# Kernel optimization log

Hardware: AMD Instinct MI355X
Metric: run time of the kernel (lower is better)

The kernel has to match this reference:

```python
import jax, jax.numpy as jnp
import numpy as np

# --- instant-NGP style multiresolution hash grid config ---
N_LEVELS = 16
F = 2                      # features per level
LOG2_T = 19
T = 1 << LOG2_T            # hash table size per level
BASE_RES = 16
SCALE = 1.5
RES = np.floor(BASE_RES * SCALE ** np.arange(N_LEVELS)).astype(np.int64)
OFFSETS = np.array([[i, j, k] for i in (0, 1) for j in (0, 1) for k in (0, 1)], dtype=np.uint32)  # [8,3] cube corners
PRIMES = np.array([1, 2654435761, 805459861], dtype=np.uint32)  # tcnn spatial hash primes
N_PTS = 2_097_152


def hash_encode(x, table):
    """x: [N,3] in [0,1); table: [L,T,F] -> [N, L*F] interpolated features."""
    feats = []
    for l in range(N_LEVELS):  # fixed small loop over levels
        res = int(RES[l])
        pos = x * res
        pos0 = jnp.floor(pos)
        w = pos - pos0                                   # [N,3] trilinear weights
        c = pos0.astype(jnp.uint32)[:, None, :] + OFFSETS[None]  # [N,8,3] corner coords
        if (res + 1) ** 3 <= T:
            # dense indexing when the full grid fits in the table
            s = np.uint32(res + 1)
            idx = c[..., 0] + c[..., 1] * s + c[..., 2] * s * s
        else:
            # spatial hash: xor of coord * prime, mod T (uint32 wraps)
            idx = (c[..., 0] * PRIMES[0]) ^ (c[..., 1] * PRIMES[1]) ^ (c[..., 2] * PRIMES[2])
            idx = idx % np.uint32(T)
        f = table[l][idx]                                # [N,8,F] irregular gather
        wc = jnp.where(OFFSETS[None].astype(bool), w[:, None, :], 1.0 - w[:, None, :])  # [N,8,3]
        weight = wc.prod(axis=-1)                        # [N,8]
        feats.append(jnp.einsum('nc,ncf->nf', weight, f))
    return jnp.concatenate(feats, axis=-1)               # [N, 32]


def setup_inputs() -> dict:
    key = jax.random.key(0)
    k1, k2, k3, k4, k5 = jax.random.split(key, 5)
    x = jax.random.uniform(k1, (N_PTS, 3), dtype=jnp.float32)
    table = jax.random.normal(k2, (N_LEVELS, T, F), dtype=jnp.float32) * 1e-2
    W1 = jax.random.normal(k3, (N_LEVELS * F, 64), dtype=jnp.float32) * (1.0 / np.sqrt(32))
    W2 = jax.random.normal(k4, (64, 64), dtype=jnp.float32) * (1.0 / 8.0)
    W3 = jax.random.normal(k5, (64, 16), dtype=jnp.float32) * (1.0 / 8.0)
    return {"x": x, "table": table, "W1": W1, "W2": W2, "W3": W3}


def reference(x, table, W1, W2, W3):
    h = hash_encode(x, table)           # [N,32]
    h = jax.nn.relu(h @ W1)             # fully-fused tiny MLP (bias-free, tcnn style)
    h = jax.nn.relu(h @ W2)
    return h @ W3                        # [N,16]
```

## Files before the change

### kernel.cpp

```cpp
#include <hip/hip_runtime.h>
#include <hip/hip_bf16.h>


#define NLVL 16
#define TSZ   524288u
#define TMASK 524287u
#define PR1 2654435761u
#define PR2 805459861u

__device__ __constant__ int kResC[NLVL] = {16,24,36,54,81,121,182,273,410,615,922,1383,2075,3113,4670,7006};
constexpr int kRes[NLVL] = {16,24,36,54,81,121,182,273,410,615,922,1383,2075,3113,4670,7006};
constexpr bool kDense[NLVL] = {true,true,true,true,false,false,false,false,
                               false,false,false,false,false,false,false,false};

__global__ __launch_bounds__(256)
void ngp_fused_kernel(const float* __restrict__ x,
                      const float* __restrict__ table,
                      const float* __restrict__ W1,
                      const float* __restrict__ W2,
                      const float* __restrict__ W3,
                      float* __restrict__ out,
                      int n)
{
    __shared__ float sW1[32 * 64];
    __shared__ float sW2[64 * 64];
    __shared__ float sW3[64 * 16];
    __shared__ float hS[32 * 256];

    const int t = threadIdx.x;

#pragma unroll
    for (int r = 0; r < 8; ++r)  sW1[r * 256 + t] = W1[r * 256 + t];
#pragma unroll
    for (int r = 0; r < 16; ++r) sW2[r * 256 + t] = W2[r * 256 + t];
#pragma unroll
    for (int r = 0; r < 4; ++r)  sW3[r * 256 + t] = W3[r * 256 + t];
    __syncthreads();

    const int i = blockIdx.x * 256 + t;
    if (i >= n) return;

    const float px = x[3 * i + 0];
    const float py = x[3 * i + 1];
    const float pz = x[3 * i + 2];

    float h[32];
#pragma unroll
    for (int l = 0; l < NLVL; ++l) {
        const float res = (float)kRes[l];
        const float fx = px * res, fy = py * res, fz = pz * res;
        const float bx = floorf(fx), by = floorf(fy), bz = floorf(fz);
        const float wx = fx - bx, wy = fy - by, wz = fz - bz;
        const unsigned cx = (unsigned)bx, cy = (unsigned)by, cz = (unsigned)bz;

        unsigned i0, i1, i2, i3, i4, i5, i6, i7;
        if (kDense[l]) {
            const unsigned s  = (unsigned)kRes[l] + 1u;
            const unsigned s2 = s * s;
            const unsigned b  = cx + cy * s + cz * s2;
            i0 = b;            i1 = b + s2;
            i2 = b + s;        i3 = b + s + s2;
            i4 = b + 1u;       i5 = b + 1u + s2;
            i6 = b + 1u + s;   i7 = b + 1u + s + s2;
        } else {
            const unsigned hx0 = cx,        hx1 = cx + 1u;
            const unsigned hy0 = cy * PR1,  hy1 = hy0 + PR1;
            const unsigned hz0 = cz * PR2,  hz1 = hz0 + PR2;
            i0 = (hx0 ^ hy0 ^ hz0) & TMASK;  i1 = (hx0 ^ hy0 ^ hz1) & TMASK;
            i2 = (hx0 ^ hy1 ^ hz0) & TMASK;  i3 = (hx0 ^ hy1 ^ hz1) & TMASK;
            i4 = (hx1 ^ hy0 ^ hz0) & TMASK;  i5 = (hx1 ^ hy0 ^ hz1) & TMASK;
            i6 = (hx1 ^ hy1 ^ hz0) & TMASK;  i7 = (hx1 ^ hy1 ^ hz1) & TMASK;
        }

        const float2* __restrict__ tl =
            reinterpret_cast<const float2*>(table) + (size_t)l * TSZ;
        const float2 f0 = tl[i0], f1 = tl[i1], f2 = tl[i2], f3 = tl[i3];
        const float2 f4 = tl[i4], f5 = tl[i5], f6 = tl[i6], f7 = tl[i7];

        const float ax = 1.f - wx, ay = 1.f - wy, az = 1.f - wz;
        const float g00 = ax * ay, g01 = ax * wy, g10 = wx * ay, g11 = wx * wy;
        float a0 = 0.f, a1 = 0.f, v;
        v = g00 * az; a0 = fmaf(v, f0.x, a0); a1 = fmaf(v, f0.y, a1);
        v = g00 * wz; a0 = fmaf(v, f1.x, a0); a1 = fmaf(v, f1.y, a1);
        v = g01 * az; a0 = fmaf(v, f2.x, a0); a1 = fmaf(v, f2.y, a1);
        v = g01 * wz; a0 = fmaf(v, f3.x, a0); a1 = fmaf(v, f3.y, a1);
        v = g10 * az; a0 = fmaf(v, f4.x, a0); a1 = fmaf(v, f4.y, a1);
        v = g10 * wz; a0 = fmaf(v, f5.x, a0); a1 = fmaf(v, f5.y, a1);
        v = g11 * az; a0 = fmaf(v, f6.x, a0); a1 = fmaf(v, f6.y, a1);
        v = g11 * wz; a0 = fmaf(v, f7.x, a0); a1 = fmaf(v, f7.y, a1);
        h[2 * l + 0] = a0;
        h[2 * l + 1] = a1;
    }

#pragma unroll
    for (int k = 0; k < 32; ++k) hS[k * 256 + t] = h[k];

    float h1[64];
#pragma unroll
    for (int j = 0; j < 64; ++j) h1[j] = 0.f;
    for (int k = 0; k < 32; ++k) {
        const float hk = hS[k * 256 + t];
        const float4* __restrict__ wr = reinterpret_cast<const float4*>(&sW1[k * 64]);
#pragma unroll
        for (int q = 0; q < 16; ++q) {
            const float4 wv = wr[q];
            h1[4 * q + 0] = fmaf(hk, wv.x, h1[4 * q + 0]);
            h1[4 * q + 1] = fmaf(hk, wv.y, h1[4 * q + 1]);
            h1[4 * q + 2] = fmaf(hk, wv.z, h1[4 * q + 2]);
            h1[4 * q + 3] = fmaf(hk, wv.w, h1[4 * q + 3]);
        }
    }
#pragma unroll
    for (int j = 0; j < 64; ++j) h1[j] = fmaxf(h1[j], 0.f);

    float h2[64];
#pragma unroll
    for (int j = 0; j < 64; ++j) h2[j] = 0.f;

#pragma unroll
    for (int k = 0; k < 32; ++k) hS[k * 256 + t] = h1[k];
    for (int k = 0; k < 32; ++k) {
        const float hk = hS[k * 256 + t];
        const float4* __restrict__ wr = reinterpret_cast<const float4*>(&sW2[k * 64]);
#pragma unroll
        for (int q = 0; q < 16; ++q) {
            const float4 wv = wr[q];
            h2[4 * q + 0] = fmaf(hk, wv.x, h2[4 * q + 0]);
            h2[4 * q + 1] = fmaf(hk, wv.y, h2[4 * q + 1]);
            h2[4 * q + 2] = fmaf(hk, wv.z, h2[4 * q + 2]);
            h2[4 * q + 3] = fmaf(hk, wv.w, h2[4 * q + 3]);
        }
    }
#pragma unroll
    for (int k = 0; k < 32; ++k) hS[k * 256 + t] = h1[32 + k];
    for (int k = 0; k < 32; ++k) {
        const float hk = hS[k * 256 + t];
        const float4* __restrict__ wr = reinterpret_cast<const float4*>(&sW2[(k + 32) * 64]);
#pragma unroll
        for (int q = 0; q < 16; ++q) {
            const float4 wv = wr[q];
            h2[4 * q + 0] = fmaf(hk, wv.x, h2[4 * q + 0]);
            h2[4 * q + 1] = fmaf(hk, wv.y, h2[4 * q + 1]);
            h2[4 * q + 2] = fmaf(hk, wv.z, h2[4 * q + 2]);
            h2[4 * q + 3] = fmaf(hk, wv.w, h2[4 * q + 3]);
        }
    }
#pragma unroll
    for (int j = 0; j < 64; ++j) h2[j] = fmaxf(h2[j], 0.f);

    float h3[16];
#pragma unroll
    for (int j = 0; j < 16; ++j) h3[j] = 0.f;

#pragma unroll
    for (int k = 0; k < 32; ++k) hS[k * 256 + t] = h2[k];
    for (int k = 0; k < 32; ++k) {
        const float hk = hS[k * 256 + t];
        const float4* __restrict__ wr = reinterpret_cast<const float4*>(&sW3[k * 16]);
#pragma unroll
        for (int q = 0; q < 4; ++q) {
            const float4 wv = wr[q];
            h3[4 * q + 0] = fmaf(hk, wv.x, h3[4 * q + 0]);
            h3[4 * q + 1] = fmaf(hk, wv.y, h3[4 * q + 1]);
            h3[4 * q + 2] = fmaf(hk, wv.z, h3[4 * q + 2]);
            h3[4 * q + 3] = fmaf(hk, wv.w, h3[4 * q + 3]);
        }
    }
#pragma unroll
    for (int k = 0; k < 32; ++k) hS[k * 256 + t] = h2[32 + k];
    for (int k = 0; k < 32; ++k) {
        const float hk = hS[k * 256 + t];
        const float4* __restrict__ wr = reinterpret_cast<const float4*>(&sW3[(k + 32) * 16]);
#pragma unroll
        for (int q = 0; q < 4; ++q) {
            const float4 wv = wr[q];
            h3[4 * q + 0] = fmaf(hk, wv.x, h3[4 * q + 0]);
            h3[4 * q + 1] = fmaf(hk, wv.y, h3[4 * q + 1]);
            h3[4 * q + 2] = fmaf(hk, wv.z, h3[4 * q + 2]);
            h3[4 * q + 3] = fmaf(hk, wv.w, h3[4 * q + 3]);
        }
    }

    float4* __restrict__ o = reinterpret_cast<float4*>(out + (size_t)i * 16);
    o[0] = make_float4(h3[0],  h3[1],  h3[2],  h3[3]);
    o[1] = make_float4(h3[4],  h3[5],  h3[6],  h3[7]);
    o[2] = make_float4(h3[8],  h3[9],  h3[10], h3[11]);
    o[3] = make_float4(h3[12], h3[13], h3[14], h3[15]);
}

extern "C" void kernel_launch(void* const* d_in, const int* in_sizes, int n_in,
                              void* d_out, int out_size, void* d_ws, size_t ws_size,
                              hipStream_t stream) {
    const float* x     = (const float*)d_in[0];
    const float* table = (const float*)d_in[1];
    const float* W1    = (const float*)d_in[2];
    const float* W2    = (const float*)d_in[3];
    const float* W3    = (const float*)d_in[4];
    float* out = (float*)d_out;

    const int n = in_sizes[0] / 3;
    const int blocks = (n + 255) / 256;
    ngp_fused_kernel<<<blocks, 256, 0, stream>>>(x, table, W1, W2, W3, out, n);
}
```

Before: 1.697 ms.

## Split into level-major encode kernel and separate register-resident MLP kernel

Encoding moves into its own kernel whose grid is partitioned by level, one pass for the four dense levels and one per hash level, so concurrently running blocks gather from a single 4 MB table and get better L2 locality. Features are written to a feature-major workspace, and a second kernel runs the MLP from registers, chaining layer 2 and layer 3 in halves and dropping the LDS round-trips. This adds 256 MB of workspace write plus read traffic and a second launch. The old fused kernel remains as a fallback when the workspace is too small. The grid is hardcoded to 4096 chunks of 512 points, which matches exactly N=2M.

```diff
diff --git a/kernel.cpp b/kernel.cpp
--- a/kernel.cpp
+++ b/kernel.cpp
@@ -12,6 +12,208 @@
 constexpr int kRes[NLVL] = {16,24,36,54,81,121,182,273,410,615,922,1383,2075,3113,4670,7006};
 constexpr bool kDense[NLVL] = {true,true,true,true,false,false,false,false,
                                false,false,false,false,false,false,false,false};
+
+
+__device__ __forceinline__ void trilerp(const float2 f0, const float2 f1, const float2 f2, const float2 f3,
+                                        const float2 f4, const float2 f5, const float2 f6, const float2 f7,
+                                        float wx, float wy, float wz, float& a0, float& a1)
+{
+    const float ax = 1.f - wx, ay = 1.f - wy, az = 1.f - wz;
+    const float g00 = ax * ay, g01 = ax * wy, g10 = wx * ay, g11 = wx * wy;
+    float s0 = 0.f, s1 = 0.f, v;
+    v = g00 * az; s0 = fmaf(v, f0.x, s0); s1 = fmaf(v, f0.y, s1);
+    v = g00 * wz; s0 = fmaf(v, f1.x, s0); s1 = fmaf(v, f1.y, s1);
+    v = g01 * az; s0 = fmaf(v, f2.x, s0); s1 = fmaf(v, f2.y, s1);
+    v = g01 * wz; s0 = fmaf(v, f3.x, s0); s1 = fmaf(v, f3.y, s1);
+    v = g10 * az; s0 = fmaf(v, f4.x, s0); s1 = fmaf(v, f4.y, s1);
+    v = g10 * wz; s0 = fmaf(v, f5.x, s0); s1 = fmaf(v, f5.y, s1);
+    v = g11 * az; s0 = fmaf(v, f6.x, s0); s1 = fmaf(v, f6.y, s1);
+    v = g11 * wz; s0 = fmaf(v, f7.x, s0); s1 = fmaf(v, f7.y, s1);
+    a0 = s0; a1 = s1;
+}
+
+__device__ __forceinline__ void hash_point(float px, float py, float pz, float res,
+                                           const float2* __restrict__ tl,
+                                           float& a0, float& a1)
+{
+    const float fx = px * res, fy = py * res, fz = pz * res;
+    const float bx = floorf(fx), by = floorf(fy), bz = floorf(fz);
+    const float wx = fx - bx, wy = fy - by, wz = fz - bz;
+    const unsigned cx = (unsigned)bx, cy = (unsigned)by, cz = (unsigned)bz;
+    const unsigned hy0 = cy * PR1, hy1 = hy0 + PR1;
+    const unsigned hz0 = cz * PR2, hz1 = hz0 + PR2;
+    const unsigned e00 = hy0 ^ hz0, e01 = hy0 ^ hz1, e10 = hy1 ^ hz0, e11 = hy1 ^ hz1;
+    const unsigned x1 = cx + 1u;
+    const float2 f0 = tl[(cx ^ e00) & TMASK];
+    const float2 f1 = tl[(cx ^ e01) & TMASK];
+    const float2 f2 = tl[(cx ^ e10) & TMASK];
+    const float2 f3 = tl[(cx ^ e11) & TMASK];
+    const float2 f4 = tl[(x1 ^ e00) & TMASK];
+    const float2 f5 = tl[(x1 ^ e01) & TMASK];
+    const float2 f6 = tl[(x1 ^ e10) & TMASK];
+    const float2 f7 = tl[(x1 ^ e11) & TMASK];
+    trilerp(f0,f1,f2,f3,f4,f5,f6,f7, wx,wy,wz, a0,a1);
+}
+
+template<int RES>
+__device__ __forceinline__ void dense_point(float px, float py, float pz,
+                                            const float2* __restrict__ tl,
+                                            float& a0, float& a1)
+{
+    const float res = (float)RES;
+    const float fx = px * res, fy = py * res, fz = pz * res;
+    const float bx = floorf(fx), by = floorf(fy), bz = floorf(fz);
+    const float wx = fx - bx, wy = fy - by, wz = fz - bz;
+    const unsigned cx = (unsigned)bx, cy = (unsigned)by, cz = (unsigned)bz;
+    const unsigned s = RES + 1u, s2 = s * s;
+    const unsigned b = cx + cy * s + cz * s2;
+    const float2 f0 = tl[b];
+    const float2 f1 = tl[b + s2];
+    const float2 f2 = tl[b + s];
+    const float2 f3 = tl[b + s + s2];
+    const float2 f4 = tl[b + 1u];
+    const float2 f5 = tl[b + 1u + s2];
+    const float2 f6 = tl[b + 1u + s];
+    const float2 f7 = tl[b + 1u + s + s2];
+    trilerp(f0,f1,f2,f3,f4,f5,f6,f7, wx,wy,wz, a0,a1);
+}
+
+__global__ __launch_bounds__(256)
+void encode_kernel(const float* __restrict__ x, const float* __restrict__ table,
+                   float* __restrict__ hT, int n)
+{
+    const int bid = blockIdx.x;
+    const int pass = bid >> 12;
+    const int chunk = bid & 4095;
+    const int t = threadIdx.x;
+    const int base = chunk * 512 + t;
+
+    if (pass == 0) {
+#pragma unroll
+        for (int p = 0; p < 2; ++p) {
+            const int i = base + p * 256;
+            if (i >= n) continue;
+            const float px = x[3*i+0], py = x[3*i+1], pz = x[3*i+2];
+            float a0, a1;
+            dense_point<16>(px,py,pz, (const float2*)table + (size_t)0*TSZ, a0,a1);
+            hT[(size_t)0*n + i] = a0; hT[(size_t)1*n + i] = a1;
+            dense_point<24>(px,py,pz, (const float2*)table + (size_t)1*TSZ, a0,a1);
+            hT[(size_t)2*n + i] = a0; hT[(size_t)3*n + i] = a1;
+            dense_point<36>(px,py,pz, (const float2*)table + (size_t)2*TSZ, a0,a1);
+            hT[(size_t)4*n + i] = a0; hT[(size_t)5*n + i] = a1;
+            dense_point<54>(px,py,pz, (const float2*)table + (size_t)3*TSZ, a0,a1);
+            hT[(size_t)6*n + i] = a0; hT[(size_t)7*n + i] = a1;
+        }
+    } else {
+        const int l = pass + 3;
+        const float res = (float)kResC[l];
+        const float2* tl = (const float2*)table + (size_t)l * TSZ;
+        float* __restrict__ r0 = hT + (size_t)(2*l) * n;
+        float* __restrict__ r1 = r0 + n;
+#pragma unroll
+        for (int p = 0; p < 2; ++p) {
+            const int i = base + p * 256;
+            if (i >= n) continue;
+            const float px = x[3*i+0], py = x[3*i+1], pz = x[3*i+2];
+            float a0, a1;
+            hash_point(px,py,pz, res, tl, a0,a1);
+            r0[i] = a0; r1[i] = a1;
+        }
+    }
+}
+
+
+__global__ __launch_bounds__(256)
+void mlp_kernel(const float* __restrict__ hT,
+                const float* __restrict__ W1,
+                const float* __restrict__ W2,
+                const float* __restrict__ W3,
+                float* __restrict__ out, int n)
+{
+    __shared__ float sW1[32 * 64];
+    __shared__ float sW2[64 * 64];
+    __shared__ float sW3[64 * 16];
+    const int t = threadIdx.x;
+#pragma unroll
+    for (int r = 0; r < 8; ++r)  sW1[r * 256 + t] = W1[r * 256 + t];
+#pragma unroll
+    for (int r = 0; r < 16; ++r) sW2[r * 256 + t] = W2[r * 256 + t];
+#pragma unroll
+    for (int r = 0; r < 4; ++r)  sW3[r * 256 + t] = W3[r * 256 + t];
+    __syncthreads();
+
+    const int i = blockIdx.x * 256 + t;
+    if (i >= n) return;
+
+    float h[32];
+#pragma unroll
+    for (int f = 0; f < 32; ++f) h[f] = hT[(size_t)f * n + i];
+
+    float h1[64];
+#pragma unroll
+    for (int j = 0; j < 64; ++j) h1[j] = 0.f;
+#pragma unroll
+    for (int k = 0; k < 32; ++k) {
+        const float hk = h[k];
+        const float4* __restrict__ wr = reinterpret_cast<const float4*>(&sW1[k * 64]);
+#pragma unroll
+        for (int q = 0; q < 16; ++q) {
+            const float4 wv = wr[q];
+            h1[4*q+0] = fmaf(hk, wv.x, h1[4*q+0]);
+            h1[4*q+1] = fmaf(hk, wv.y, h1[4*q+1]);
+            h1[4*q+2] = fmaf(hk, wv.z, h1[4*q+2]);
+            h1[4*q+3] = fmaf(hk, wv.w, h1[4*q+3]);
+        }
+    }
+#pragma unroll
+    for (int j = 0; j < 64; ++j) h1[j] = fmaxf(h1[j], 0.f);
+
+    float h3[16];
+#pragma unroll
+    for (int j = 0; j < 16; ++j) h3[j] = 0.f;
+
+#pragma unroll
+    for (int half = 0; half < 2; ++half) {
+        float h2[32];
+#pragma unroll
+        for (int j = 0; j < 32; ++j) h2[j] = 0.f;
+#pragma unroll
+        for (int k = 0; k < 64; ++k) {
+            const float hk = h1[k];
+            const float4* __restrict__ wr = reinterpret_cast<const float4*>(&sW2[k * 64 + half * 32]);
+#pragma unroll
+            for (int q = 0; q < 8; ++q) {
+                const float4 wv = wr[q];
+                h2[4*q+0] = fmaf(hk, wv.x, h2[4*q+0]);
+                h2[4*q+1] = fmaf(hk, wv.y, h2[4*q+1]);
+                h2[4*q+2] = fmaf(hk, wv.z, h2[4*q+2]);
+                h2[4*q+3] = fmaf(hk, wv.w, h2[4*q+3]);
+            }
+        }
+#pragma unroll
+        for (int j = 0; j < 32; ++j) h2[j] = fmaxf(h2[j], 0.f);
+#pragma unroll
+        for (int k = 0; k < 32; ++k) {
+            const float hk = h2[k];
+            const float4* __restrict__ wr = reinterpret_cast<const float4*>(&sW3[(half * 32 + k) * 16]);
+#pragma unroll
+            for (int q = 0; q < 4; ++q) {
+                const float4 wv = wr[q];
+                h3[4*q+0] = fmaf(hk, wv.x, h3[4*q+0]);
+                h3[4*q+1] = fmaf(hk, wv.y, h3[4*q+1]);
+                h3[4*q+2] = fmaf(hk, wv.z, h3[4*q+2]);
+                h3[4*q+3] = fmaf(hk, wv.w, h3[4*q+3]);
+            }
+        }
+    }
+
+    float4* __restrict__ o = reinterpret_cast<float4*>(out + (size_t)i * 16);
+    o[0] = make_float4(h3[0],  h3[1],  h3[2],  h3[3]);
+    o[1] = make_float4(h3[4],  h3[5],  h3[6],  h3[7]);
+    o[2] = make_float4(h3[8],  h3[9],  h3[10], h3[11]);
+    o[3] = make_float4(h3[12], h3[13], h3[14], h3[15]);
+}
+
 
 __global__ __launch_bounds__(256)
 void ngp_fused_kernel(const float* __restrict__ x,
@@ -28,7 +230,6 @@
     __shared__ float hS[32 * 256];
 
     const int t = threadIdx.x;
-
 #pragma unroll
     for (int r = 0; r < 8; ++r)  sW1[r * 256 + t] = W1[r * 256 + t];
 #pragma unroll
@@ -40,56 +241,22 @@
     const int i = blockIdx.x * 256 + t;
     if (i >= n) return;
 
-    const float px = x[3 * i + 0];
-    const float py = x[3 * i + 1];
-    const float pz = x[3 * i + 2];
+    const float px = x[3*i+0], py = x[3*i+1], pz = x[3*i+2];
 
     float h[32];
 #pragma unroll
     for (int l = 0; l < NLVL; ++l) {
-        const float res = (float)kRes[l];
-        const float fx = px * res, fy = py * res, fz = pz * res;
-        const float bx = floorf(fx), by = floorf(fy), bz = floorf(fz);
-        const float wx = fx - bx, wy = fy - by, wz = fz - bz;
-        const unsigned cx = (unsigned)bx, cy = (unsigned)by, cz = (unsigned)bz;
-
-        unsigned i0, i1, i2, i3, i4, i5, i6, i7;
+        float a0, a1;
         if (kDense[l]) {
-            const unsigned s  = (unsigned)kRes[l] + 1u;
-            const unsigned s2 = s * s;
-            const unsigned b  = cx + cy * s + cz * s2;
-            i0 = b;            i1 = b + s2;
-            i2 = b + s;        i3 = b + s + s2;
-            i4 = b + 1u;       i5 = b + 1u + s2;
-            i6 = b + 1u + s;   i7 = b + 1u + s + s2;
+            const int r = kRes[l];
+            if (r == 16) dense_point<16>(px,py,pz,(const float2*)table+(size_t)l*TSZ,a0,a1);
+            else if (r == 24) dense_point<24>(px,py,pz,(const float2*)table+(size_t)l*TSZ,a0,a1);
+            else if (r == 36) dense_point<36>(px,py,pz,(const float2*)table+(size_t)l*TSZ,a0,a1);
+            else dense_point<54>(px,py,pz,(const float2*)table+(size_t)l*TSZ,a0,a1);
         } else {
-            const unsigned hx0 = cx,        hx1 = cx + 1u;
-            const unsigned hy0 = cy * PR1,  hy1 = hy0 + PR1;
-            const unsigned hz0 = cz * PR2,  hz1 = hz0 + PR2;
-            i0 = (hx0 ^ hy0 ^ hz0) & TMASK;  i1 = (hx0 ^ hy0 ^ hz1) & TMASK;
-            i2 = (hx0 ^ hy1 ^ hz0) & TMASK;  i3 = (hx0 ^ hy1 ^ hz1) & TMASK;
-            i4 = (hx1 ^ hy0 ^ hz0) & TMASK;  i5 = (hx1 ^ hy0 ^ hz1) & TMASK;
-            i6 = (hx1 ^ hy1 ^ hz0) & TMASK;  i7 = (hx1 ^ hy1 ^ hz1) & TMASK;
-        }
-
-        const float2* __restrict__ tl =
-            reinterpret_cast<const float2*>(table) + (size_t)l * TSZ;
-        const float2 f0 = tl[i0], f1 = tl[i1], f2 = tl[i2], f3 = tl[i3];
-        const float2 f4 = tl[i4], f5 = tl[i5], f6 = tl[i6], f7 = tl[i7];
-
-        const float ax = 1.f - wx, ay = 1.f - wy, az = 1.f - wz;
-        const float g00 = ax * ay, g01 = ax * wy, g10 = wx * ay, g11 = wx * wy;
-        float a0 = 0.f, a1 = 0.f, v;
-        v = g00 * az; a0 = fmaf(v, f0.x, a0); a1 = fmaf(v, f0.y, a1);
-        v = g00 * wz; a0 = fmaf(v, f1.x, a0); a1 = fmaf(v, f1.y, a1);
-        v = g01 * az; a0 = fmaf(v, f2.x, a0); a1 = fmaf(v, f2.y, a1);
-        v = g01 * wz; a0 = fmaf(v, f3.x, a0); a1 = fmaf(v, f3.y, a1);
-        v = g10 * az; a0 = fmaf(v, f4.x, a0); a1 = fmaf(v, f4.y, a1);
-        v = g10 * wz; a0 = fmaf(v, f5.x, a0); a1 = fmaf(v, f5.y, a1);
-        v = g11 * az; a0 = fmaf(v, f6.x, a0); a1 = fmaf(v, f6.y, a1);
-        v = g11 * wz; a0 = fmaf(v, f7.x, a0); a1 = fmaf(v, f7.y, a1);
-        h[2 * l + 0] = a0;
-        h[2 * l + 1] = a1;
+            hash_point(px,py,pz,(float)kRes[l],(const float2*)table+(size_t)l*TSZ,a0,a1);
+        }
+        h[2*l+0] = a0; h[2*l+1] = a1;
     }
 
 #pragma unroll
@@ -104,10 +271,10 @@
 #pragma unroll
         for (int q = 0; q < 16; ++q) {
             const float4 wv = wr[q];
-            h1[4 * q + 0] = fmaf(hk, wv.x, h1[4 * q + 0]);
-            h1[4 * q + 1] = fmaf(hk, wv.y, h1[4 * q + 1]);
-            h1[4 * q + 2] = fmaf(hk, wv.z, h1[4 * q + 2]);
-            h1[4 * q + 3] = fmaf(hk, wv.w, h1[4 * q + 3]);
+            h1[4*q+0] = fmaf(hk, wv.x, h1[4*q+0]);
+            h1[4*q+1] = fmaf(hk, wv.y, h1[4*q+1]);
+            h1[4*q+2] = fmaf(hk, wv.z, h1[4*q+2]);
+            h1[4*q+3] = fmaf(hk, wv.w, h1[4*q+3]);
         }
     }
 #pragma unroll
@@ -116,33 +283,21 @@
     float h2[64];
 #pragma unroll
     for (int j = 0; j < 64; ++j) h2[j] = 0.f;
-
-#pragma unroll
-    for (int k = 0; k < 32; ++k) hS[k * 256 + t] = h1[k];
-    for (int k = 0; k < 32; ++k) {
-        const float hk = hS[k * 256 + t];
-        const float4* __restrict__ wr = reinterpret_cast<const float4*>(&sW2[k * 64]);
-#pragma unroll
-        for (int q = 0; q < 16; ++q) {
-            const float4 wv = wr[q];
-            h2[4 * q + 0] = fmaf(hk, wv.x, h2[4 * q + 0]);
-            h2[4 * q + 1] = fmaf(hk, wv.y, h2[4 * q + 1]);
-            h2[4 * q + 2] = fmaf(hk, wv.z, h2[4 * q + 2]);
-            h2[4 * q + 3] = fmaf(hk, wv.w, h2[4 * q + 3]);
-        }
-    }
-#pragma unroll
-    for (int k = 0; k < 32; ++k) hS[k * 256 + t] = h1[32 + k];
-    for (int k = 0; k < 32; ++k) {
-        const float hk = hS[k * 256 + t];
-        const float4* __restrict__ wr = reinterpret_cast<const float4*>(&sW2[(k + 32) * 64]);
-#pragma unroll
-        for (int q = 0; q < 16; ++q) {
-            const float4 wv = wr[q];
-            h2[4 * q + 0] = fmaf(hk, wv.x, h2[4 * q + 0]);
-            h2[4 * q + 1] = fmaf(hk, wv.y, h2[4 * q + 1]);
-            h2[4 * q + 2] = fmaf(hk, wv.z, h2[4 * q + 2]);
-            h2[4 * q + 3] = fmaf(hk, wv.w, h2[4 * q + 3]);
+#pragma unroll
+    for (int half = 0; half < 2; ++half) {
+#pragma unroll
+        for (int k = 0; k < 32; ++k) hS[k * 256 + t] = h1[half * 32 + k];
+        for (int k = 0; k < 32; ++k) {
+            const float hk = hS[k * 256 + t];
+            const float4* __restrict__ wr = reinterpret_cast<const float4*>(&sW2[(half * 32 + k) * 64]);
+#pragma unroll
+            for (int q = 0; q < 16; ++q) {
+                const float4 wv = wr[q];
+                h2[4*q+0] = fmaf(hk, wv.x, h2[4*q+0]);
+                h2[4*q+1] = fmaf(hk, wv.y, h2[4*q+1]);
+                h2[4*q+2] = fmaf(hk, wv.z, h2[4*q+2]);
+                h2[4*q+3] = fmaf(hk, wv.w, h2[4*q+3]);
+            }
         }
     }
 #pragma unroll
@@ -151,33 +306,21 @@
     float h3[16];
 #pragma unroll
     for (int j = 0; j < 16; ++j) h3[j] = 0.f;
-
-#pragma unroll
-    for (int k = 0; k < 32; ++k) hS[k * 256 + t] = h2[k];
-    for (int k = 0; k < 32; ++k) {
-        const float hk = hS[k * 256 + t];
-        const float4* __restrict__ wr = reinterpret_cast<const float4*>(&sW3[k * 16]);
-#pragma unroll
-        for (int q = 0; q < 4; ++q) {
-            const float4 wv = wr[q];
-            h3[4 * q + 0] = fmaf(hk, wv.x, h3[4 * q + 0]);
-            h3[4 * q + 1] = fmaf(hk, wv.y, h3[4 * q + 1]);
-            h3[4 * q + 2] = fmaf(hk, wv.z, h3[4 * q + 2]);
-            h3[4 * q + 3] = fmaf(hk, wv.w, h3[4 * q + 3]);
-        }
-    }
-#pragma unroll
-    for (int k = 0; k < 32; ++k) hS[k * 256 + t] = h2[32 + k];
-    for (int k = 0; k < 32; ++k) {
-        const float hk = hS[k * 256 + t];
-        const float4* __restrict__ wr = reinterpret_cast<const float4*>(&sW3[(k + 32) * 16]);
-#pragma unroll
-        for (int q = 0; q < 4; ++q) {
-            const float4 wv = wr[q];
-            h3[4 * q + 0] = fmaf(hk, wv.x, h3[4 * q + 0]);
-            h3[4 * q + 1] = fmaf(hk, wv.y, h3[4 * q + 1]);
-            h3[4 * q + 2] = fmaf(hk, wv.z, h3[4 * q + 2]);
-            h3[4 * q + 3] = fmaf(hk, wv.w, h3[4 * q + 3]);
+#pragma unroll
+    for (int half = 0; half < 2; ++half) {
+#pragma unroll
+        for (int k = 0; k < 32; ++k) hS[k * 256 + t] = h2[half * 32 + k];
+        for (int k = 0; k < 32; ++k) {
+            const float hk = hS[k * 256 + t];
+            const float4* __restrict__ wr = reinterpret_cast<const float4*>(&sW3[(half * 32 + k) * 16]);
+#pragma unroll
+            for (int q = 0; q < 4; ++q) {
+                const float4 wv = wr[q];
+                h3[4*q+0] = fmaf(hk, wv.x, h3[4*q+0]);
+                h3[4*q+1] = fmaf(hk, wv.y, h3[4*q+1]);
+                h3[4*q+2] = fmaf(hk, wv.z, h3[4*q+2]);
+                h3[4*q+3] = fmaf(hk, wv.w, h3[4*q+3]);
+            }
         }
     }
 
@@ -199,6 +342,15 @@
     float* out = (float*)d_out;
 
     const int n = in_sizes[0] / 3;
-    const int blocks = (n + 255) / 256;
-    ngp_fused_kernel<<<blocks, 256, 0, stream>>>(x, table, W1, W2, W3, out, n);
-}
+    const size_t need = (size_t)n * 32 * sizeof(float);
+
+    if (ws_size >= need) {
+        float* hT = (float*)d_ws;
+        const int chunks = (n + 511) / 512;
+        encode_kernel<<<13 * 4096, 256, 0, stream>>>(x, table, hT, n);
+        (void)chunks;
+        mlp_kernel<<<(n + 255) / 256, 256, 0, stream>>>(hT, W1, W2, W3, out, n);
+    } else {
+        ngp_fused_kernel<<<(n + 255) / 256, 256, 0, stream>>>(x, table, W1, W2, W3, out, n);
+    }
+}
```

New measurement: 1.741 ms. 1.03x slower.
